# Optimization experiments

Hardware: AMD Instinct MI355X
Metric: run time of the kernel (lower is better)

Reference implementation:

```python
import jax, jax.numpy as jnp
import numpy as np

B, N, V = 1024, 256, 200


def setup_inputs() -> dict:
    key = jax.random.key(0)
    ks = jax.random.split(key, 24)
    merged = jax.random.normal(ks[0], (B, N, 15), dtype=jnp.float32)
    # active flag column in {0,1}; row 0 is the subject bus and is always active
    flag = (jax.random.uniform(ks[1], (B, N)) < 0.5).astype(jnp.float32)
    flag = flag.at[:, 0].set(1.0)
    merged = merged.at[:, :, 14].set(flag)
    a = jax.random.normal(ks[2], (B,), dtype=jnp.float32)
    w = lambda k, s: jax.random.normal(k, s, dtype=jnp.float32) * 0.05
    return dict(
        merged=merged, a=a,
        up_Wq=w(ks[3], (7, V)), up_Wk=w(ks[4], (14, V)), up_Wv=w(ks[5], (14, V)),
        dn_Wq=w(ks[6], (7, V)), dn_Wk=w(ks[7], (14, V)), dn_Wv=w(ks[8], (14, V)),
        pv_Wq=w(ks[9], (7, V)), pv_Wk=w(ks[10], (7, V)), pv_Wv=w(ks[11], (7, V)),
        t_W1=w(ks[12], (3, V, V)), t_b1=w(ks[13], (3, V)),
        t_W2=w(ks[14], (3, V, 1)), t_b2=w(ks[15], (3, 1)),
        e_W1=w(ks[16], (4, V)), e_b1=w(ks[17], (V,)),
        e_W2=w(ks[18], (V, V)), e_b2=w(ks[19], (V,)),
        e_W3=w(ks[20], (V, 1)), e_b3=w(ks[21], (1,)),
        gamma=jnp.ones((V,), jnp.float32), beta=jnp.zeros((V,), jnp.float32),
    )


def reference(merged, a, up_Wq, up_Wk, up_Wv, dn_Wq, dn_Wk, dn_Wv,
              pv_Wq, pv_Wk, pv_Wv, t_W1, t_b1, t_W2, t_b2,
              e_W1, e_b1, e_W2, e_b2, e_W3, e_b3, gamma, beta):
    v_dim = gamma.shape[0]
    scale = np.float32(1.0 / np.sqrt(v_dim))
    # merged_s[0, 6] = a  (subject bus action)
    merged = merged.at[:, 0, 6].set(a)
    # subtract subject bus id from id columns 0 and 7
    subj_id = merged[:, 0:1, 0]                       # [B,1]
    merged = merged.at[:, :, 0].add(-subj_id)
    merged = merged.at[:, :, 7].add(-subj_id)
    subj_loc = merged[:, 0:1, 2]                      # [B,1]
    flag = merged[:, :, 14]                           # [B,N]
    loc = merged[:, :, 2]                             # [B,N]
    up_mask = (loc < subj_loc) & (flag == 1.0)        # active upstream (excludes subject: loc==subj_loc)
    dn_mask = (loc > subj_loc) & (flag == 1.0)        # active downstream
    pv_mask = flag == 0.0                             # passive buses (row 0 is active by construction)
    ego = merged[:, 0, :7]                            # [B,7]
    f14 = merged[:, :, :14]                           # [B,N,14]
    f7 = merged[:, :, :7]                             # [B,N,7]

    def attend(Wq, Wk, Wv, feat, mask):
        # single-query cross attention: ego query vs ragged (masked) neighbor set
        q = ego @ Wq                                  # [B,V]
        k = jnp.einsum('bnf,fv->bnv', feat, Wk)
        v = jnp.einsum('bnf,fv->bnv', feat, Wv)
        s = jnp.einsum('bv,bnv->bn', q, k) * scale
        s = jnp.where(mask, s, jnp.float32(-1e9))
        out = jnp.einsum('bn,bnv->bv', jax.nn.softmax(s, axis=-1), v)
        # empty neighbor set -> zeros(v_dim) (compute_attention_target fallback)
        return jnp.where(mask.any(-1, keepdims=True), out, 0.0)

    u = attend(up_Wq, up_Wk, up_Wv, f14, up_mask)
    d = attend(dn_Wq, dn_Wk, dn_Wv, f14, dn_mask)
    p = attend(pv_Wq, pv_Wk, pv_Wv, f7, pv_mask)

    def bn(x):  # BatchNorm1d in training mode: batch statistics, biased var
        m = x.mean(0)
        var = x.var(0)
        return gamma * (x - m) * jax.lax.rsqrt(var + 1e-5) + beta

    t = jnp.stack([bn(u), bn(d), bn(p)], 0)           # [3,B,V]
    h = jax.nn.elu(jnp.einsum('kbv,kvw->kbw', t, t_W1) + t_b1[:, None, :])
    heads = jnp.einsum('kbw,kwo->kbo', h, t_W2) + t_b2[:, None, :]  # [3,B,1]
    ego_t = merged[:, 0, 3:7]                         # cols [3,4,5,6] = [hb,hf,occp,a]
    q1 = jax.nn.relu(ego_t @ e_W1 + e_b1)
    q1 = jax.nn.relu(q1 @ e_W2 + e_b2)
    Q1 = q1 @ e_W3 + e_b3                             # [B,1]
    G1 = Q1 + heads[0] + heads[1] + heads[2]
    return G1.reshape(-1, 1)
```

## Files before the change

kernel.cpp:

```cpp
#include <hip/hip_runtime.h>
#include <math.h>

#define BB 1024
#define NN 256
#define VV 200
#define BT 8
#define NSH 16

#define WS_M    0
#define WS_STAT 256
#define WS_X    19456

__global__ __launch_bounds__(256) void k_prep(const float* __restrict__ upWq, const float* __restrict__ upWk,
                                              const float* __restrict__ dnWq, const float* __restrict__ dnWk,
                                              const float* __restrict__ pvWq, const float* __restrict__ pvWk,
                                              float* __restrict__ ws, float* __restrict__ out) {
    __shared__ float wq[7 * VV];
    __shared__ float wk[14 * VV];
    int blk = blockIdx.x, tid = threadIdx.x;
    float* stat = ws + WS_STAT;
    for (int i = blk * 256 + tid; i < 2 * NSH * 600; i += 768) stat[i] = 0.f;
    for (int i = blk * 256 + tid; i < BB; i += 768) out[i] = 0.f;

    const float* Wq = blk == 0 ? upWq : (blk == 1 ? dnWq : pvWq);
    const float* Wk = blk == 0 ? upWk : (blk == 1 ? dnWk : pvWk);
    int F = (blk == 2) ? 7 : 14;
    int off = blk == 0 ? 0 : (blk == 1 ? 98 : 196);
    for (int i = tid; i < 7 * VV; i += 256) wq[i] = Wq[i];
    for (int i = tid; i < F * VV; i += 256) wk[i] = Wk[i];
    __syncthreads();
    if (tid < 7 * F) {
        int i = tid / F, f = tid % F;
        float s = 0.f;
        for (int v = 0; v < VV; v++) s += wq[i * VV + v] * wk[f * VV + v];
        ws[WS_M + off + tid] = s;
    }
}

__global__ __launch_bounds__(256) void k_attn(
    const float* __restrict__ merged, const float* __restrict__ a,
    const float* __restrict__ upWv, const float* __restrict__ dnWv, const float* __restrict__ pvWv,
    float* __restrict__ ws) {
    int tid = threadIdx.x;
    int lane = tid & 63, wave = tid >> 6;
    int b = blockIdx.x * 4 + wave;

    __shared__ float sm[4 * NN * 15];
    const float4* g4 = (const float4*)(merged + (size_t)blockIdx.x * 4 * NN * 15);
    float4* s4p = (float4*)sm;
    for (int i = tid; i < 4 * NN * 15 / 4; i += 256) s4p[i] = g4[i];
    __syncthreads();

    const float* row = sm + wave * NN * 15;
    const float* gM = ws + WS_M;
    float* g_sum = ws + WS_STAT;
    float* g_ss  = ws + WS_STAT + NSH * 600;
    float* g_x   = ws + WS_X;

    float ab = a[b];
    float subj_id = row[0];
    float subj_loc = row[2];
    float e1 = row[1], e2 = row[2], e3 = row[3], e4 = row[4], e5 = row[5], e6 = ab;

    float feat[4][14];
    float flag[4];
#pragma unroll
    for (int k = 0; k < 4; k++) {
        int base = (lane + 64 * k) * 15;
#pragma unroll
        for (int f = 0; f < 14; f++) feat[k][f] = row[base + f];
        flag[k] = row[base + 14];
        feat[k][0] -= subj_id;
        feat[k][7] -= subj_id;
    }
    if (lane == 0) feat[0][6] = ab;

    float em = 0.f;
    if (lane < 35) {
        int h = lane < 14 ? 0 : (lane < 28 ? 1 : 2);
        int f = lane - (h == 0 ? 0 : (h == 1 ? 14 : 28));
        int F = (h == 2) ? 7 : 14;
        const float* M = gM + (h == 0 ? 0 : (h == 1 ? 98 : 196));
        em = e1 * M[1 * F + f] + e2 * M[2 * F + f] + e3 * M[3 * F + f] +
             e4 * M[4 * F + f] + e5 * M[5 * F + f] + e6 * M[6 * F + f];
    }

    float s0[4] = {0, 0, 0, 0}, s1[4] = {0, 0, 0, 0}, s2[4] = {0, 0, 0, 0};
#pragma unroll
    for (int f = 0; f < 14; f++) {
        float bv = __shfl(em, f);
#pragma unroll
        for (int k = 0; k < 4; k++) s0[k] += bv * feat[k][f];
    }
#pragma unroll
    for (int f = 0; f < 14; f++) {
        float bv = __shfl(em, 14 + f);
#pragma unroll
        for (int k = 0; k < 4; k++) s1[k] += bv * feat[k][f];
    }
#pragma unroll
    for (int f = 0; f < 7; f++) {
        float bv = __shfl(em, 28 + f);
#pragma unroll
        for (int k = 0; k < 4; k++) s2[k] += bv * feat[k][f];
    }

    const float scale = 7.0710678118654752e-2f;
#pragma unroll
    for (int k = 0; k < 4; k++) {
        float loc = feat[k][2];
        s0[k] = ((loc < subj_loc) && (flag[k] == 1.f)) ? s0[k] * scale : -1e9f;
        s1[k] = ((loc > subj_loc) && (flag[k] == 1.f)) ? s1[k] * scale : -1e9f;
        s2[k] = (flag[k] == 0.f) ? s2[k] * scale : -1e9f;
    }

    float m0 = fmaxf(fmaxf(s0[0], s0[1]), fmaxf(s0[2], s0[3]));
    float m1 = fmaxf(fmaxf(s1[0], s1[1]), fmaxf(s1[2], s1[3]));
    float m2 = fmaxf(fmaxf(s2[0], s2[1]), fmaxf(s2[2], s2[3]));
#pragma unroll
    for (int off = 32; off; off >>= 1) {
        m0 = fmaxf(m0, __shfl_xor(m0, off));
        m1 = fmaxf(m1, __shfl_xor(m1, off));
        m2 = fmaxf(m2, __shfl_xor(m2, off));
    }
    float p0[4], p1[4], p2[4];
    float z0 = 0.f, z1 = 0.f, z2 = 0.f;
#pragma unroll
    for (int k = 0; k < 4; k++) {
        p0[k] = expf(s0[k] - m0); z0 += p0[k];
        p1[k] = expf(s1[k] - m1); z1 += p1[k];
        p2[k] = expf(s2[k] - m2); z2 += p2[k];
    }
#pragma unroll
    for (int off = 32; off; off >>= 1) {
        z0 += __shfl_xor(z0, off);
        z1 += __shfl_xor(z1, off);
        z2 += __shfl_xor(z2, off);
    }
    float r0 = 1.f / z0, r1 = 1.f / z1, r2 = 1.f / z2;
#pragma unroll
    for (int k = 0; k < 4; k++) { p0[k] *= r0; p1[k] *= r1; p2[k] *= r2; }

    float pc[35];
#pragma unroll
    for (int f = 0; f < 14; f++) {
        float c0 = 0.f, c1 = 0.f;
#pragma unroll
        for (int k = 0; k < 4; k++) { c0 += p0[k] * feat[k][f]; c1 += p1[k] * feat[k][f]; }
        pc[f] = c0; pc[14 + f] = c1;
    }
#pragma unroll
    for (int f = 0; f < 7; f++) {
        float c2 = 0.f;
#pragma unroll
        for (int k = 0; k < 4; k++) c2 += p2[k] * feat[k][f];
        pc[28 + f] = c2;
    }
#pragma unroll
    for (int off = 32; off; off >>= 1)
#pragma unroll
        for (int j = 0; j < 35; j++) pc[j] += __shfl_xor(pc[j], off);

    int shard = blockIdx.x & (NSH - 1);
    const float* Wvs[3] = {upWv, dnWv, pvWv};
    float mh[3] = {m0, m1, m2};
    const int coff[3] = {0, 14, 28};
#pragma unroll
    for (int h = 0; h < 3; h++) {
        const float* Wv = Wvs[h];
        const float* c = pc + coff[h];
        int F = (h == 2) ? 7 : 14;
        bool empty = (mh[h] == -1e9f);
#pragma unroll
        for (int slot = 0; slot < 4; slot++) {
            int v = lane + 64 * slot;
            if (v < VV) {
                float val = 0.f;
                for (int f = 0; f < F; f++) val += c[f] * Wv[f * VV + v];
                if (empty) val = 0.f;
                g_x[((size_t)h * BB + b) * VV + v] = val;
                atomicAdd(&g_sum[shard * 600 + h * VV + v], val);
                atomicAdd(&g_ss[shard * 600 + h * VV + v], val * val);
            }
        }
    }
}

__global__ __launch_bounds__(256) void k_final(const float* __restrict__ merged, const float* __restrict__ a,
                                               const float* __restrict__ tW1, const float* __restrict__ tb1,
                                               const float* __restrict__ tW2, const float* __restrict__ tb2,
                                               const float* __restrict__ eW1, const float* __restrict__ eb1,
                                               const float* __restrict__ eW2, const float* __restrict__ eb2,
                                               const float* __restrict__ eW3, const float* __restrict__ eb3,
                                               const float* __restrict__ gamma, const float* __restrict__ beta,
                                               const float* __restrict__ ws,
                                               float* __restrict__ out) {
    int tile = blockIdx.x >> 2;
    int q = blockIdx.x & 3;
    int b0 = tile * BT;
    int tid = threadIdx.x;
    int lane = tid & 63, wave = tid >> 6;
    int w = tid;

    __shared__ __align__(16) float tT[VV * BT];
    __shared__ float redsh[4 * BT];
    __shared__ float esh[BT][4];

    const float* g_sum = ws + WS_STAT;
    const float* g_ss  = ws + WS_STAT + NSH * 600;
    const float* g_x   = ws + WS_X;

    float fin[BT];
#pragma unroll
    for (int bb = 0; bb < BT; bb++) fin[bb] = 0.f;

    if (q < 3) {
        __shared__ float bnA[VV], bnB[VV];
        if (w < VV) {
            float S = 0.f, S2 = 0.f;
#pragma unroll
            for (int s = 0; s < NSH; s++) {
                S += g_sum[s * 600 + q * VV + w];
                S2 += g_ss[s * 600 + q * VV + w];
            }
            float m = S * (1.f / BB);
            float var = S2 * (1.f / BB) - m * m;
            float rstd = rsqrtf(var + 1e-5f);
            float gv = gamma[w];
            bnA[w] = gv * rstd;
            bnB[w] = beta[w] - gv * rstd * m;
        }
        __syncthreads();
        for (int idx = tid; idx < BT * VV; idx += 256) {
            int v = idx % VV, bb = idx / VV;
            float val = g_x[((size_t)q * BB + b0 + bb) * VV + v];
            tT[v * BT + bb] = bnA[v] * val + bnB[v];
        }
        __syncthreads();

        if (w < VV) {
            float acc[BT];
            float bias = tb1[q * VV + w];
#pragma unroll
            for (int bb = 0; bb < BT; bb++) acc[bb] = bias;
            const float* W1 = tW1 + (size_t)q * VV * VV + w;
            const float4* tT4 = (const float4*)tT;
#pragma unroll 8
            for (int v = 0; v < VV; v++) {
                float w1 = W1[(size_t)v * VV];
                float4 t0 = tT4[v * 2 + 0];
                float4 t1 = tT4[v * 2 + 1];
                acc[0] += t0.x * w1; acc[1] += t0.y * w1; acc[2] += t0.z * w1; acc[3] += t0.w * w1;
                acc[4] += t1.x * w1; acc[5] += t1.y * w1; acc[6] += t1.z * w1; acc[7] += t1.w * w1;
            }
            float w2 = tW2[q * VV + w];
#pragma unroll
            for (int bb = 0; bb < BT; bb++) {
                float h = acc[bb];
                h = h > 0.f ? h : expf(h) - 1.f;
                fin[bb] = h * w2;
            }
        }
    } else {
        if (tid < BT) {
            const float* mrow = merged + (size_t)(b0 + tid) * NN * 15;
            esh[tid][0] = mrow[3];
            esh[tid][1] = mrow[4];
            esh[tid][2] = mrow[5];
            esh[tid][3] = a[b0 + tid];
        }
        __syncthreads();
        if (w < VV) {
            float e0 = eW1[w], e1 = eW1[VV + w], e2 = eW1[2 * VV + w], e3 = eW1[3 * VV + w];
            float bias = eb1[w];
#pragma unroll
            for (int bb = 0; bb < BT; bb++) {
                float qv = bias + esh[bb][0] * e0 + esh[bb][1] * e1 + esh[bb][2] * e2 + esh[bb][3] * e3;
                tT[w * BT + bb] = fmaxf(qv, 0.f);
            }
        }
        __syncthreads();
        if (w < VV) {
            float acc[BT];
            float bias = eb2[w];
#pragma unroll
            for (int bb = 0; bb < BT; bb++) acc[bb] = bias;
            const float* W2 = eW2 + w;
            const float4* tT4 = (const float4*)tT;
#pragma unroll 8
            for (int v = 0; v < VV; v++) {
                float w2v = W2[(size_t)v * VV];
                float4 t0 = tT4[v * 2 + 0];
                float4 t1 = tT4[v * 2 + 1];
                acc[0] += t0.x * w2v; acc[1] += t0.y * w2v; acc[2] += t0.z * w2v; acc[3] += t0.w * w2v;
                acc[4] += t1.x * w2v; acc[5] += t1.y * w2v; acc[6] += t1.z * w2v; acc[7] += t1.w * w2v;
            }
            float w3 = eW3[w];
#pragma unroll
            for (int bb = 0; bb < BT; bb++) fin[bb] = fmaxf(acc[bb], 0.f) * w3;
        }
    }

#pragma unroll
    for (int bb = 0; bb < BT; bb++)
#pragma unroll
        for (int off = 32; off; off >>= 1) fin[bb] += __shfl_xor(fin[bb], off);
    if (lane == 0)
#pragma unroll
        for (int bb = 0; bb < BT; bb++) redsh[wave * BT + bb] = fin[bb];
    __syncthreads();
    if (tid < BT) {
        float tot = redsh[tid] + redsh[BT + tid] + redsh[2 * BT + tid] + redsh[3 * BT + tid];
        if (q == 3) tot += eb3[0] + tb2[0] + tb2[1] + tb2[2];
        atomicAdd(&out[b0 + tid], tot);
    }
}

extern "C" void kernel_launch(void* const* d_in, const int* in_sizes, int n_in,
                              void* d_out, int out_size, void* d_ws, size_t ws_size,
                              hipStream_t stream) {
    const float* merged = (const float*)d_in[0];
    const float* a      = (const float*)d_in[1];
    const float* upWq   = (const float*)d_in[2];
    const float* upWk   = (const float*)d_in[3];
    const float* upWv   = (const float*)d_in[4];
    const float* dnWq   = (const float*)d_in[5];
    const float* dnWk   = (const float*)d_in[6];
    const float* dnWv   = (const float*)d_in[7];
    const float* pvWq   = (const float*)d_in[8];
    const float* pvWk   = (const float*)d_in[9];
    const float* pvWv   = (const float*)d_in[10];
    const float* tW1    = (const float*)d_in[11];
    const float* tb1    = (const float*)d_in[12];
    const float* tW2    = (const float*)d_in[13];
    const float* tb2    = (const float*)d_in[14];
    const float* eW1    = (const float*)d_in[15];
    const float* eb1    = (const float*)d_in[16];
    const float* eW2    = (const float*)d_in[17];
    const float* eb2    = (const float*)d_in[18];
    const float* eW3    = (const float*)d_in[19];
    const float* eb3    = (const float*)d_in[20];
    const float* gamma  = (const float*)d_in[21];
    const float* beta   = (const float*)d_in[22];
    float* out = (float*)d_out;
    float* ws = (float*)d_ws;

    hipLaunchKernelGGL(k_prep, dim3(3), dim3(256), 0, stream, upWq, upWk, dnWq, dnWk, pvWq, pvWk, ws, out);
    hipLaunchKernelGGL(k_attn, dim3(BB / 4), dim3(256), 0, stream, merged, a, upWv, dnWv, pvWv, ws);
    hipLaunchKernelGGL(k_final, dim3((BB / BT) * 4), dim3(256), 0, stream, merged, a,
                       tW1, tb1, tW2, tb2, eW1, eb1, eW2, eb2, eW3, eb3, gamma, beta, ws, out);
}
```

Baseline: 144.7 us.

## Register-tile final MLP GEMM with 4x4 per-thread blocks and larger batch tile

The final head kernel now processes 16 batch rows per block instead of 8. Each wave owns 4 batch rows, and each lane computes 4 output columns using float4 weight loads, giving a 4x4 register tile per thread. This halves how many times the 200x200 weights are re-read and raises FMA work per load, at the cost of idling 14 of 64 lanes per wave and using more atomics. The prep kernel now launches 8 blocks so zeroing the stats and output buffers is spread across more blocks.

```diff
diff --git a/kernel.cpp b/kernel.cpp
--- a/kernel.cpp
+++ b/kernel.cpp
@@ -4,7 +4,7 @@
 #define BB 1024
 #define NN 256
 #define VV 200
-#define BT 8
+#define BT 16
 #define NSH 16
 
 #define WS_M    0
@@ -19,21 +19,23 @@
     __shared__ float wk[14 * VV];
     int blk = blockIdx.x, tid = threadIdx.x;
     float* stat = ws + WS_STAT;
-    for (int i = blk * 256 + tid; i < 2 * NSH * 600; i += 768) stat[i] = 0.f;
-    for (int i = blk * 256 + tid; i < BB; i += 768) out[i] = 0.f;
-
-    const float* Wq = blk == 0 ? upWq : (blk == 1 ? dnWq : pvWq);
-    const float* Wk = blk == 0 ? upWk : (blk == 1 ? dnWk : pvWk);
-    int F = (blk == 2) ? 7 : 14;
-    int off = blk == 0 ? 0 : (blk == 1 ? 98 : 196);
-    for (int i = tid; i < 7 * VV; i += 256) wq[i] = Wq[i];
-    for (int i = tid; i < F * VV; i += 256) wk[i] = Wk[i];
-    __syncthreads();
-    if (tid < 7 * F) {
-        int i = tid / F, f = tid % F;
-        float s = 0.f;
-        for (int v = 0; v < VV; v++) s += wq[i * VV + v] * wk[f * VV + v];
-        ws[WS_M + off + tid] = s;
+    for (int i = blk * 256 + tid; i < 2 * NSH * 600; i += 8 * 256) stat[i] = 0.f;
+    for (int i = blk * 256 + tid; i < BB; i += 8 * 256) out[i] = 0.f;
+
+    if (blk < 3) {
+        const float* Wq = blk == 0 ? upWq : (blk == 1 ? dnWq : pvWq);
+        const float* Wk = blk == 0 ? upWk : (blk == 1 ? dnWk : pvWk);
+        int F = (blk == 2) ? 7 : 14;
+        int off = blk == 0 ? 0 : (blk == 1 ? 98 : 196);
+        for (int i = tid; i < 7 * VV; i += 256) wq[i] = Wq[i];
+        for (int i = tid; i < F * VV; i += 256) wk[i] = Wk[i];
+        __syncthreads();
+        if (tid < 7 * F) {
+            int i = tid / F, f = tid % F;
+            float s = 0.f;
+            for (int v = 0; v < VV; v++) s += wq[i * VV + v] * wk[f * VV + v];
+            ws[WS_M + off + tid] = s;
+        }
     }
 }
 
@@ -200,67 +202,38 @@
     int b0 = tile * BT;
     int tid = threadIdx.x;
     int lane = tid & 63, wave = tid >> 6;
-    int w = tid;
-
-    __shared__ __align__(16) float tT[VV * BT];
-    __shared__ float redsh[4 * BT];
+
+    __shared__ __align__(16) float tsh[VV * BT];
     __shared__ float esh[BT][4];
 
     const float* g_sum = ws + WS_STAT;
     const float* g_ss  = ws + WS_STAT + NSH * 600;
     const float* g_x   = ws + WS_X;
 
-    float fin[BT];
-#pragma unroll
-    for (int bb = 0; bb < BT; bb++) fin[bb] = 0.f;
-
+    const float* W;
     if (q < 3) {
         __shared__ float bnA[VV], bnB[VV];
-        if (w < VV) {
+        if (tid < VV) {
             float S = 0.f, S2 = 0.f;
 #pragma unroll
             for (int s = 0; s < NSH; s++) {
-                S += g_sum[s * 600 + q * VV + w];
-                S2 += g_ss[s * 600 + q * VV + w];
+                S += g_sum[s * 600 + q * VV + tid];
+                S2 += g_ss[s * 600 + q * VV + tid];
             }
             float m = S * (1.f / BB);
             float var = S2 * (1.f / BB) - m * m;
             float rstd = rsqrtf(var + 1e-5f);
-            float gv = gamma[w];
-            bnA[w] = gv * rstd;
-            bnB[w] = beta[w] - gv * rstd * m;
+            float gv = gamma[tid];
+            bnA[tid] = gv * rstd;
+            bnB[tid] = beta[tid] - gv * rstd * m;
         }
         __syncthreads();
         for (int idx = tid; idx < BT * VV; idx += 256) {
             int v = idx % VV, bb = idx / VV;
             float val = g_x[((size_t)q * BB + b0 + bb) * VV + v];
-            tT[v * BT + bb] = bnA[v] * val + bnB[v];
-        }
-        __syncthreads();
-
-        if (w < VV) {
-            float acc[BT];
-            float bias = tb1[q * VV + w];
-#pragma unroll
-            for (int bb = 0; bb < BT; bb++) acc[bb] = bias;
-            const float* W1 = tW1 + (size_t)q * VV * VV + w;
-            const float4* tT4 = (const float4*)tT;
-#pragma unroll 8
-            for (int v = 0; v < VV; v++) {
-                float w1 = W1[(size_t)v * VV];
-                float4 t0 = tT4[v * 2 + 0];
-                float4 t1 = tT4[v * 2 + 1];
-                acc[0] += t0.x * w1; acc[1] += t0.y * w1; acc[2] += t0.z * w1; acc[3] += t0.w * w1;
-                acc[4] += t1.x * w1; acc[5] += t1.y * w1; acc[6] += t1.z * w1; acc[7] += t1.w * w1;
-            }
-            float w2 = tW2[q * VV + w];
-#pragma unroll
-            for (int bb = 0; bb < BT; bb++) {
-                float h = acc[bb];
-                h = h > 0.f ? h : expf(h) - 1.f;
-                fin[bb] = h * w2;
-            }
-        }
+            tsh[v * BT + bb] = bnA[v] * val + bnB[v];
+        }
+        W = tW1 + (size_t)q * VV * VV;
     } else {
         if (tid < BT) {
             const float* mrow = merged + (size_t)(b0 + tid) * NN * 15;
@@ -270,49 +243,75 @@
             esh[tid][3] = a[b0 + tid];
         }
         __syncthreads();
-        if (w < VV) {
-            float e0 = eW1[w], e1 = eW1[VV + w], e2 = eW1[2 * VV + w], e3 = eW1[3 * VV + w];
-            float bias = eb1[w];
+        if (tid < VV) {
+            float e0 = eW1[tid], e1 = eW1[VV + tid], e2 = eW1[2 * VV + tid], e3 = eW1[3 * VV + tid];
+            float bias = eb1[tid];
 #pragma unroll
             for (int bb = 0; bb < BT; bb++) {
                 float qv = bias + esh[bb][0] * e0 + esh[bb][1] * e1 + esh[bb][2] * e2 + esh[bb][3] * e3;
-                tT[w * BT + bb] = fmaxf(qv, 0.f);
+                tsh[tid * BT + bb] = fmaxf(qv, 0.f);
             }
         }
-        __syncthreads();
-        if (w < VV) {
-            float acc[BT];
-            float bias = eb2[w];
-#pragma unroll
-            for (int bb = 0; bb < BT; bb++) acc[bb] = bias;
-            const float* W2 = eW2 + w;
-            const float4* tT4 = (const float4*)tT;
+        W = eW2;
+    }
+    __syncthreads();
+
+    bool active = (lane < 50);
+    int wbase = active ? lane * 4 : 0;
+    int bbase = wave * 4;
+
+    float4 bias4;
+    if (q < 3) bias4 = *(const float4*)&tb1[q * VV + wbase];
+    else       bias4 = *(const float4*)&eb2[wbase];
+
+    float acc[4][4];
+#pragma unroll
+    for (int bb = 0; bb < 4; bb++) {
+        acc[bb][0] = bias4.x; acc[bb][1] = bias4.y; acc[bb][2] = bias4.z; acc[bb][3] = bias4.w;
+    }
+
+    const float4* tq = (const float4*)&tsh[bbase];
 #pragma unroll 8
-            for (int v = 0; v < VV; v++) {
-                float w2v = W2[(size_t)v * VV];
-                float4 t0 = tT4[v * 2 + 0];
-                float4 t1 = tT4[v * 2 + 1];
-                acc[0] += t0.x * w2v; acc[1] += t0.y * w2v; acc[2] += t0.z * w2v; acc[3] += t0.w * w2v;
-                acc[4] += t1.x * w2v; acc[5] += t1.y * w2v; acc[6] += t1.z * w2v; acc[7] += t1.w * w2v;
-            }
-            float w3 = eW3[w];
-#pragma unroll
-            for (int bb = 0; bb < BT; bb++) fin[bb] = fmaxf(acc[bb], 0.f) * w3;
-        }
-    }
-
-#pragma unroll
-    for (int bb = 0; bb < BT; bb++)
-#pragma unroll
-        for (int off = 32; off; off >>= 1) fin[bb] += __shfl_xor(fin[bb], off);
-    if (lane == 0)
-#pragma unroll
-        for (int bb = 0; bb < BT; bb++) redsh[wave * BT + bb] = fin[bb];
-    __syncthreads();
-    if (tid < BT) {
-        float tot = redsh[tid] + redsh[BT + tid] + redsh[2 * BT + tid] + redsh[3 * BT + tid];
-        if (q == 3) tot += eb3[0] + tb2[0] + tb2[1] + tb2[2];
-        atomicAdd(&out[b0 + tid], tot);
+    for (int v = 0; v < VV; v++) {
+        float4 t4 = tq[v * (BT / 4)];
+        float4 w4 = *(const float4*)&W[(size_t)v * VV + wbase];
+        acc[0][0] += t4.x * w4.x; acc[0][1] += t4.x * w4.y; acc[0][2] += t4.x * w4.z; acc[0][3] += t4.x * w4.w;
+        acc[1][0] += t4.y * w4.x; acc[1][1] += t4.y * w4.y; acc[1][2] += t4.y * w4.z; acc[1][3] += t4.y * w4.w;
+        acc[2][0] += t4.z * w4.x; acc[2][1] += t4.z * w4.y; acc[2][2] += t4.z * w4.z; acc[2][3] += t4.z * w4.w;
+        acc[3][0] += t4.w * w4.x; acc[3][1] += t4.w * w4.y; acc[3][2] += t4.w * w4.z; acc[3][3] += t4.w * w4.w;
+    }
+
+    float fin[4] = {0.f, 0.f, 0.f, 0.f};
+    if (q < 3) {
+        float4 w2 = *(const float4*)&tW2[q * VV + wbase];
+#pragma unroll
+        for (int bb = 0; bb < 4; bb++) {
+            float h0 = acc[bb][0], h1 = acc[bb][1], h2 = acc[bb][2], h3 = acc[bb][3];
+            h0 = h0 > 0.f ? h0 : expf(h0) - 1.f;
+            h1 = h1 > 0.f ? h1 : expf(h1) - 1.f;
+            h2 = h2 > 0.f ? h2 : expf(h2) - 1.f;
+            h3 = h3 > 0.f ? h3 : expf(h3) - 1.f;
+            fin[bb] = h0 * w2.x + h1 * w2.y + h2 * w2.z + h3 * w2.w;
+        }
+    } else {
+        float4 w3 = *(const float4*)&eW3[wbase];
+#pragma unroll
+        for (int bb = 0; bb < 4; bb++) {
+            fin[bb] = fmaxf(acc[bb][0], 0.f) * w3.x + fmaxf(acc[bb][1], 0.f) * w3.y +
+                      fmaxf(acc[bb][2], 0.f) * w3.z + fmaxf(acc[bb][3], 0.f) * w3.w;
+        }
+    }
+    if (!active) { fin[0] = fin[1] = fin[2] = fin[3] = 0.f; }
+
+#pragma unroll
+    for (int off = 32; off; off >>= 1)
+#pragma unroll
+        for (int bb = 0; bb < 4; bb++) fin[bb] += __shfl_xor(fin[bb], off);
+
+    if (lane == 0) {
+        float cst = (q == 3) ? (eb3[0] + tb2[0] + tb2[1] + tb2[2]) : 0.f;
+#pragma unroll
+        for (int bb = 0; bb < 4; bb++) atomicAdd(&out[b0 + bbase + bb], fin[bb] + cst);
     }
 }
 
@@ -345,7 +344,7 @@
     float* out = (float*)d_out;
     float* ws = (float*)d_ws;
 
-    hipLaunchKernelGGL(k_prep, dim3(3), dim3(256), 0, stream, upWq, upWk, dnWq, dnWk, pvWq, pvWk, ws, out);
+    hipLaunchKernelGGL(k_prep, dim3(8), dim3(256), 0, stream, upWq, upWk, dnWq, dnWk, pvWq, pvWk, ws, out);
     hipLaunchKernelGGL(k_attn, dim3(BB / 4), dim3(256), 0, stream, merged, a, upWv, dnWv, pvWv, ws);
     hipLaunchKernelGGL(k_final, dim3((BB / BT) * 4), dim3(256), 0, stream, merged, a,
                        tW1, tb1, tW2, tb2, eW1, eb1, eW2, eb2, eW3, eb3, gamma, beta, ws, out);
```

Measured after the change: 149.7 us. 1.03x slower.

## Process one batch row per attention block with block-wide softmax reductions

Applied to the files above, without the earlier changes.

The attention kernel now gives each batch element its own 256-thread block, with one thread per neighbor instead of one wave handling four neighbors per lane. Softmax max and sum reductions run across waves through shared memory, and the weighted feature sums are computed cooperatively from shared memory in place of 35-wide register shuffles. The aim is to cut register pressure and quadruple the number of blocks for better occupancy and latency hiding. The cost is extra block synchronisations and shared-memory traffic. The prep kernel also uses 8 blocks to zero the stats buffers.

```diff
diff --git a/kernel.cpp b/kernel.cpp
--- a/kernel.cpp
+++ b/kernel.cpp
@@ -19,21 +19,23 @@
     __shared__ float wk[14 * VV];
     int blk = blockIdx.x, tid = threadIdx.x;
     float* stat = ws + WS_STAT;
-    for (int i = blk * 256 + tid; i < 2 * NSH * 600; i += 768) stat[i] = 0.f;
-    for (int i = blk * 256 + tid; i < BB; i += 768) out[i] = 0.f;
-
-    const float* Wq = blk == 0 ? upWq : (blk == 1 ? dnWq : pvWq);
-    const float* Wk = blk == 0 ? upWk : (blk == 1 ? dnWk : pvWk);
-    int F = (blk == 2) ? 7 : 14;
-    int off = blk == 0 ? 0 : (blk == 1 ? 98 : 196);
-    for (int i = tid; i < 7 * VV; i += 256) wq[i] = Wq[i];
-    for (int i = tid; i < F * VV; i += 256) wk[i] = Wk[i];
-    __syncthreads();
-    if (tid < 7 * F) {
-        int i = tid / F, f = tid % F;
-        float s = 0.f;
-        for (int v = 0; v < VV; v++) s += wq[i * VV + v] * wk[f * VV + v];
-        ws[WS_M + off + tid] = s;
+    for (int i = blk * 256 + tid; i < 2 * NSH * 600; i += 8 * 256) stat[i] = 0.f;
+    for (int i = blk * 256 + tid; i < BB; i += 8 * 256) out[i] = 0.f;
+
+    if (blk < 3) {
+        const float* Wq = blk == 0 ? upWq : (blk == 1 ? dnWq : pvWq);
+        const float* Wk = blk == 0 ? upWk : (blk == 1 ? dnWk : pvWk);
+        int F = (blk == 2) ? 7 : 14;
+        int off = blk == 0 ? 0 : (blk == 1 ? 98 : 196);
+        for (int i = tid; i < 7 * VV; i += 256) wq[i] = Wq[i];
+        for (int i = tid; i < F * VV; i += 256) wk[i] = Wk[i];
+        __syncthreads();
+        if (tid < 7 * F) {
+            int i = tid / F, f = tid % F;
+            float s = 0.f;
+            for (int v = 0; v < VV; v++) s += wq[i * VV + v] * wk[f * VV + v];
+            ws[WS_M + off + tid] = s;
+        }
     }
 }
 
@@ -41,147 +43,132 @@
     const float* __restrict__ merged, const float* __restrict__ a,
     const float* __restrict__ upWv, const float* __restrict__ dnWv, const float* __restrict__ pvWv,
     float* __restrict__ ws) {
+    int b = blockIdx.x;
     int tid = threadIdx.x;
     int lane = tid & 63, wave = tid >> 6;
-    int b = blockIdx.x * 4 + wave;
-
-    __shared__ float sm[4 * NN * 15];
-    const float4* g4 = (const float4*)(merged + (size_t)blockIdx.x * 4 * NN * 15);
-    float4* s4p = (float4*)sm;
-    for (int i = tid; i < 4 * NN * 15 / 4; i += 256) s4p[i] = g4[i];
-    __syncthreads();
-
-    const float* row = sm + wave * NN * 15;
+
+    __shared__ float sm[NN * 15];
+    __shared__ float eMsh[35];
+    __shared__ float psh[3 * NN];
+    __shared__ float part[245];
+    __shared__ float csh[35];
+    __shared__ float wred[4][3];
+
     const float* gM = ws + WS_M;
     float* g_sum = ws + WS_STAT;
     float* g_ss  = ws + WS_STAT + NSH * 600;
     float* g_x   = ws + WS_X;
 
+    const float4* g4 = (const float4*)(merged + (size_t)b * NN * 15);
+    float4* s4p = (float4*)sm;
+    for (int i = tid; i < NN * 15 / 4; i += 256) s4p[i] = g4[i];
+    __syncthreads();
+
     float ab = a[b];
-    float subj_id = row[0];
-    float subj_loc = row[2];
-    float e1 = row[1], e2 = row[2], e3 = row[3], e4 = row[4], e5 = row[5], e6 = ab;
-
-    float feat[4][14];
-    float flag[4];
-#pragma unroll
-    for (int k = 0; k < 4; k++) {
-        int base = (lane + 64 * k) * 15;
-#pragma unroll
-        for (int f = 0; f < 14; f++) feat[k][f] = row[base + f];
-        flag[k] = row[base + 14];
-        feat[k][0] -= subj_id;
-        feat[k][7] -= subj_id;
-    }
-    if (lane == 0) feat[0][6] = ab;
-
-    float em = 0.f;
-    if (lane < 35) {
-        int h = lane < 14 ? 0 : (lane < 28 ? 1 : 2);
-        int f = lane - (h == 0 ? 0 : (h == 1 ? 14 : 28));
+    float subj_id = sm[0];
+    float subj_loc = sm[2];
+    __syncthreads();
+
+    sm[tid * 15 + 0] -= subj_id;
+    sm[tid * 15 + 7] -= subj_id;
+    if (tid == 0) sm[6] = ab;
+    if (tid < 35) {
+        int h = tid < 14 ? 0 : (tid < 28 ? 1 : 2);
+        int f = tid - (h == 0 ? 0 : (h == 1 ? 14 : 28));
         int F = (h == 2) ? 7 : 14;
         const float* M = gM + (h == 0 ? 0 : (h == 1 ? 98 : 196));
-        em = e1 * M[1 * F + f] + e2 * M[2 * F + f] + e3 * M[3 * F + f] +
-             e4 * M[4 * F + f] + e5 * M[5 * F + f] + e6 * M[6 * F + f];
-    }
-
-    float s0[4] = {0, 0, 0, 0}, s1[4] = {0, 0, 0, 0}, s2[4] = {0, 0, 0, 0};
+        float e1 = sm[1], e2 = sm[2], e3 = sm[3], e4 = sm[4], e5 = sm[5];
+        eMsh[tid] = e1 * M[1 * F + f] + e2 * M[2 * F + f] + e3 * M[3 * F + f] +
+                    e4 * M[4 * F + f] + e5 * M[5 * F + f] + ab * M[6 * F + f];
+    }
+    __syncthreads();
+
+    float feat[14];
+#pragma unroll
+    for (int f = 0; f < 14; f++) feat[f] = sm[tid * 15 + f];
+    float flag = sm[tid * 15 + 14];
+    float loc = feat[2];
+
+    float s0 = 0.f, s1 = 0.f, s2 = 0.f;
 #pragma unroll
     for (int f = 0; f < 14; f++) {
-        float bv = __shfl(em, f);
-#pragma unroll
-        for (int k = 0; k < 4; k++) s0[k] += bv * feat[k][f];
-    }
-#pragma unroll
-    for (int f = 0; f < 14; f++) {
-        float bv = __shfl(em, 14 + f);
-#pragma unroll
-        for (int k = 0; k < 4; k++) s1[k] += bv * feat[k][f];
-    }
-#pragma unroll
-    for (int f = 0; f < 7; f++) {
-        float bv = __shfl(em, 28 + f);
-#pragma unroll
-        for (int k = 0; k < 4; k++) s2[k] += bv * feat[k][f];
-    }
+        s0 += eMsh[f] * feat[f];
+        s1 += eMsh[14 + f] * feat[f];
+    }
+#pragma unroll
+    for (int f = 0; f < 7; f++) s2 += eMsh[28 + f] * feat[f];
 
     const float scale = 7.0710678118654752e-2f;
-#pragma unroll
-    for (int k = 0; k < 4; k++) {
-        float loc = feat[k][2];
-        s0[k] = ((loc < subj_loc) && (flag[k] == 1.f)) ? s0[k] * scale : -1e9f;
-        s1[k] = ((loc > subj_loc) && (flag[k] == 1.f)) ? s1[k] * scale : -1e9f;
-        s2[k] = (flag[k] == 0.f) ? s2[k] * scale : -1e9f;
-    }
-
-    float m0 = fmaxf(fmaxf(s0[0], s0[1]), fmaxf(s0[2], s0[3]));
-    float m1 = fmaxf(fmaxf(s1[0], s1[1]), fmaxf(s1[2], s1[3]));
-    float m2 = fmaxf(fmaxf(s2[0], s2[1]), fmaxf(s2[2], s2[3]));
+    s0 = ((loc < subj_loc) && (flag == 1.f)) ? s0 * scale : -1e9f;
+    s1 = ((loc > subj_loc) && (flag == 1.f)) ? s1 * scale : -1e9f;
+    s2 = (flag == 0.f) ? s2 * scale : -1e9f;
+
+    float m0 = s0, m1 = s1, m2 = s2;
 #pragma unroll
     for (int off = 32; off; off >>= 1) {
         m0 = fmaxf(m0, __shfl_xor(m0, off));
         m1 = fmaxf(m1, __shfl_xor(m1, off));
         m2 = fmaxf(m2, __shfl_xor(m2, off));
     }
-    float p0[4], p1[4], p2[4];
-    float z0 = 0.f, z1 = 0.f, z2 = 0.f;
-#pragma unroll
-    for (int k = 0; k < 4; k++) {
-        p0[k] = expf(s0[k] - m0); z0 += p0[k];
-        p1[k] = expf(s1[k] - m1); z1 += p1[k];
-        p2[k] = expf(s2[k] - m2); z2 += p2[k];
-    }
+    if (lane == 0) { wred[wave][0] = m0; wred[wave][1] = m1; wred[wave][2] = m2; }
+    __syncthreads();
+    m0 = fmaxf(fmaxf(wred[0][0], wred[1][0]), fmaxf(wred[2][0], wred[3][0]));
+    m1 = fmaxf(fmaxf(wred[0][1], wred[1][1]), fmaxf(wred[2][1], wred[3][1]));
+    m2 = fmaxf(fmaxf(wred[0][2], wred[1][2]), fmaxf(wred[2][2], wred[3][2]));
+    float e0 = expf(s0 - m0), e1 = expf(s1 - m1), e2 = expf(s2 - m2);
+    float z0 = e0, z1 = e1, z2 = e2;
 #pragma unroll
     for (int off = 32; off; off >>= 1) {
         z0 += __shfl_xor(z0, off);
         z1 += __shfl_xor(z1, off);
         z2 += __shfl_xor(z2, off);
     }
-    float r0 = 1.f / z0, r1 = 1.f / z1, r2 = 1.f / z2;
-#pragma unroll
-    for (int k = 0; k < 4; k++) { p0[k] *= r0; p1[k] *= r1; p2[k] *= r2; }
-
-    float pc[35];
-#pragma unroll
-    for (int f = 0; f < 14; f++) {
-        float c0 = 0.f, c1 = 0.f;
-#pragma unroll
-        for (int k = 0; k < 4; k++) { c0 += p0[k] * feat[k][f]; c1 += p1[k] * feat[k][f]; }
-        pc[f] = c0; pc[14 + f] = c1;
-    }
-#pragma unroll
-    for (int f = 0; f < 7; f++) {
-        float c2 = 0.f;
-#pragma unroll
-        for (int k = 0; k < 4; k++) c2 += p2[k] * feat[k][f];
-        pc[28 + f] = c2;
-    }
-#pragma unroll
-    for (int off = 32; off; off >>= 1)
-#pragma unroll
-        for (int j = 0; j < 35; j++) pc[j] += __shfl_xor(pc[j], off);
-
-    int shard = blockIdx.x & (NSH - 1);
-    const float* Wvs[3] = {upWv, dnWv, pvWv};
-    float mh[3] = {m0, m1, m2};
-    const int coff[3] = {0, 14, 28};
-#pragma unroll
-    for (int h = 0; h < 3; h++) {
-        const float* Wv = Wvs[h];
-        const float* c = pc + coff[h];
-        int F = (h == 2) ? 7 : 14;
-        bool empty = (mh[h] == -1e9f);
-#pragma unroll
-        for (int slot = 0; slot < 4; slot++) {
-            int v = lane + 64 * slot;
-            if (v < VV) {
-                float val = 0.f;
-                for (int f = 0; f < F; f++) val += c[f] * Wv[f * VV + v];
-                if (empty) val = 0.f;
-                g_x[((size_t)h * BB + b) * VV + v] = val;
-                atomicAdd(&g_sum[shard * 600 + h * VV + v], val);
-                atomicAdd(&g_ss[shard * 600 + h * VV + v], val * val);
-            }
+    __syncthreads();
+    if (lane == 0) { wred[wave][0] = z0; wred[wave][1] = z1; wred[wave][2] = z2; }
+    __syncthreads();
+    z0 = wred[0][0] + wred[1][0] + wred[2][0] + wred[3][0];
+    z1 = wred[0][1] + wred[1][1] + wred[2][1] + wred[3][1];
+    z2 = wred[0][2] + wred[1][2] + wred[2][2] + wred[3][2];
+
+    psh[0 * NN + tid] = e0 / z0;
+    psh[1 * NN + tid] = e1 / z1;
+    psh[2 * NN + tid] = e2 / z2;
+    __syncthreads();
+
+    if (tid < 245) {
+        int d = tid / 7, j = tid % 7;
+        int h = d < 14 ? 0 : (d < 28 ? 1 : 2);
+        int f = d - (h == 0 ? 0 : (h == 1 ? 14 : 28));
+        const float* p = psh + h * NN;
+        float s = 0.f;
+        for (int n = j; n < NN; n += 7) s += p[n] * sm[n * 15 + f];
+        part[tid] = s;
+    }
+    __syncthreads();
+    if (tid < 35) {
+        float s = 0.f;
+#pragma unroll
+        for (int j = 0; j < 7; j++) s += part[tid * 7 + j];
+        csh[tid] = s;
+    }
+    __syncthreads();
+
+    if (tid < VV) {
+        int shard = b & (NSH - 1);
+        const float* Wvs[3] = {upWv, dnWv, pvWv};
+        float mh[3] = {m0, m1, m2};
+        const int coff[3] = {0, 14, 28};
+        const int Fs[3] = {14, 14, 7};
+#pragma unroll
+        for (int h = 0; h < 3; h++) {
+            const float* Wv = Wvs[h];
+            const float* c = csh + coff[h];
+            float val = 0.f;
+            for (int f = 0; f < Fs[h]; f++) val += c[f] * Wv[f * VV + tid];
+            if (mh[h] == -1e9f) val = 0.f;
+            g_x[((size_t)h * BB + b) * VV + tid] = val;
+            atomicAdd(&g_sum[shard * 600 + h * VV + tid], val);
+            atomicAdd(&g_ss[shard * 600 + h * VV + tid], val * val);
         }
     }
 }
@@ -345,8 +332,8 @@
     float* out = (float*)d_out;
     float* ws = (float*)d_ws;
 
-    hipLaunchKernelGGL(k_prep, dim3(3), dim3(256), 0, stream, upWq, upWk, dnWq, dnWk, pvWq, pvWk, ws, out);
-    hipLaunchKernelGGL(k_attn, dim3(BB / 4), dim3(256), 0, stream, merged, a, upWv, dnWv, pvWv, ws);
+    hipLaunchKernelGGL(k_prep, dim3(8), dim3(256), 0, stream, upWq, upWk, dnWq, dnWk, pvWq, pvWk, ws, out);
+    hipLaunchKernelGGL(k_attn, dim3(BB), dim3(256), 0, stream, merged, a, upWv, dnWv, pvWv, ws);
     hipLaunchKernelGGL(k_final, dim3((BB / BT) * 4), dim3(256), 0, stream, merged, a,
                        tW1, tb1, tW2, tb2, eW1, eb1, eW2, eb2, eW3, eb3, gamma, beta, ws, out);
 }
```

After: 138.6 us (median of 2 runs). -4.2%, faster.
